# Performance work log

Measured on AMD Instinct MI355X. Metric: run time of the kernel, lower is better.

The kernel has to match this reference:

```python
import jax, jax.numpy as jnp
import numpy as np

THETA = 10000.0
B, S, D, H = 2, 2048, 1024, 16
DK = D // H


def setup_inputs() -> dict:
    key = jax.random.key(0)
    ks = jax.random.split(key, 5)
    std = float(np.sqrt(2.0 / (D + D)))  # get_std(in, out) with in==out==D
    x = jax.random.normal(ks[0], (B, S, D), dtype=jnp.float32)
    Wq = jax.random.normal(ks[1], (D, D), dtype=jnp.float32) * std
    Wk = jax.random.normal(ks[2], (D, D), dtype=jnp.float32) * std
    Wv = jax.random.normal(ks[3], (D, D), dtype=jnp.float32) * std
    Wo = jax.random.normal(ks[4], (D, D), dtype=jnp.float32) * std
    token_positions = jnp.broadcast_to(jnp.arange(S, dtype=jnp.int32), (B, S))
    return {"x": x, "Wq": Wq, "Wk": Wk, "Wv": Wv, "Wo": Wo,
            "token_positions": token_positions}


def _rope(x, pos):
    # x: [B, H, S, d] with interleaved pairs (even=x1, odd=x2); pos: [B, 1, S]
    d = x.shape[-1]
    inv_freq = THETA ** (-(jnp.arange(0, d, 2, dtype=jnp.float32) / d))  # [d/2]
    freqs = pos[..., None].astype(jnp.float32) * inv_freq               # [B,1,S,d/2]
    cos, sin = jnp.cos(freqs), jnp.sin(freqs)
    x1, x2 = x[..., 0::2], x[..., 1::2]
    r1 = cos * x1 - sin * x2
    r2 = sin * x1 + cos * x2
    return jnp.stack([r1, r2], axis=-1).reshape(x.shape)  # re-interleave


def reference(x, Wq, Wk, Wv, Wo, token_positions):
    # Linear is y = x @ W.T (torch weight layout [out, in])
    def split_heads(t):
        return t.reshape(B, S, H, DK).transpose(0, 2, 1, 3)  # [B,H,S,DK]

    Q = split_heads(x @ Wq.T)
    K = split_heads(x @ Wk.T)
    V = split_heads(x @ Wv.T)

    pos = token_positions[:, None, :]  # [B,1,S] broadcast over heads
    Q = _rope(Q, pos)
    K = _rope(K, pos)

    scale = 1.0 / jnp.sqrt(jnp.float32(DK))
    scores = jnp.einsum('bhqd,bhkd->bhqk', Q, K) * scale  # [B,H,S,S]
    causal = jnp.arange(S)[:, None] >= jnp.arange(S)[None, :]
    scores = jnp.where(causal, scores, -jnp.inf)
    weights = jax.nn.softmax(scores, axis=-1)
    attn = jnp.einsum('bhqk,bhkd->bhqd', weights, V)
    attn = attn.transpose(0, 2, 1, 3).reshape(B, S, D)
    return attn @ Wo.T
```

## Files before the change

### kernel.cpp

```cpp
#include <hip/hip_runtime.h>
#include <hip/hip_bf16.h>
#include <math.h>

#define B_ 2
#define S_ 2048
#define D_ 1024
#define H_ 16
#define DK_ 64

typedef __bf16 bf16_t;
typedef bf16_t bf16x8 __attribute__((ext_vector_type(8)));
typedef bf16_t bf16x4 __attribute__((ext_vector_type(4)));
typedef float f32x4 __attribute__((ext_vector_type(4)));

__device__ __forceinline__ void gload16(const void* g, void* lds_base_uniform) {
  __builtin_amdgcn_global_load_lds(
      (const __attribute__((address_space(1))) unsigned int*)g,
      (__attribute__((address_space(3))) unsigned int*)lds_base_uniform, 16, 0, 0);
}

__global__ __launch_bounds__(256) void cast_bf16_vec(const float* __restrict__ in,
                                                     bf16_t* __restrict__ out, int n4) {
  int i = blockIdx.x * 256 + threadIdx.x;
  if (i >= n4) return;
  float4 f = reinterpret_cast<const float4*>(in)[i];
  bf16x4 o;
  o[0] = (bf16_t)f.x; o[1] = (bf16_t)f.y; o[2] = (bf16_t)f.z; o[3] = (bf16_t)f.w;
  reinterpret_cast<bf16x4*>(out)[i] = o;
}

__global__ __launch_bounds__(256) void cast_weights(const float* __restrict__ Wq,
                                                    const float* __restrict__ Wk,
                                                    const float* __restrict__ Wv,
                                                    const float* __restrict__ Wo,
                                                    bf16_t* __restrict__ out) {
  int i = blockIdx.x * 256 + threadIdx.x;
  int r = i >> 18;
  const float* src = (r == 0) ? Wq : (r == 1) ? Wk : (r == 2) ? Wv : Wo;
  float4 f = reinterpret_cast<const float4*>(src)[i & 262143];
  bf16x4 o;
  o[0] = (bf16_t)f.x; o[1] = (bf16_t)f.y; o[2] = (bf16_t)f.z; o[3] = (bf16_t)f.w;
  reinterpret_cast<bf16x4*>(out)[i] = o;
}

template <bool OUT_F32>
__global__ __launch_bounds__(512) void gemm_bt(const bf16_t* __restrict__ A,
                                               const bf16_t* __restrict__ W,
                                               void* __restrict__ Cout,
                                               int Ndim, int Kdim) {
  __shared__ __attribute__((aligned(16))) bf16_t As[128][64];
  __shared__ __attribute__((aligned(16))) bf16_t Bs[128][64];
  const int bm = blockIdx.x * 128;
  const int bn = blockIdx.y * 128;
  const int tid = threadIdx.x;
  const int lane = tid & 63;
  const int w = tid >> 6;
  const int wm = w >> 2, wn = w & 3;
  const int srow_c = lane >> 3;
  const int sslot = lane & 7;

  f32x4 acc[4][2];
  for (int m = 0; m < 4; ++m)
    for (int n = 0; n < 2; ++n) acc[m][n] = (f32x4){0.f, 0.f, 0.f, 0.f};

  for (int k0 = 0; k0 < Kdim; k0 += 64) {
    __syncthreads();
#pragma unroll
    for (int it = 0; it < 2; ++it) {
      const int c = 2 * w + it;
      const int row = c * 8 + srow_c;
      const int col = ((sslot ^ (row & 7)) << 3);
      gload16(&A[(size_t)(bm + row) * Kdim + k0 + col], (char*)&As[0][0] + c * 1024);
      gload16(&W[(size_t)(bn + row) * Kdim + k0 + col], (char*)&Bs[0][0] + c * 1024);
    }
    __syncthreads();
#pragma unroll
    for (int t = 0; t < 2; ++t) {
      const int slot0 = t * 4 + (lane >> 4);
      bf16x8 af[4], bfr[2];
#pragma unroll
      for (int m = 0; m < 4; ++m) {
        const int R = wm * 64 + m * 16 + (lane & 15);
        af[m] = *reinterpret_cast<const bf16x8*>(
            (const char*)&As[0][0] + R * 128 + ((slot0 ^ (R & 7)) << 4));
      }
#pragma unroll
      for (int n = 0; n < 2; ++n) {
        const int R = wn * 32 + n * 16 + (lane & 15);
        bfr[n] = *reinterpret_cast<const bf16x8*>(
            (const char*)&Bs[0][0] + R * 128 + ((slot0 ^ (R & 7)) << 4));
      }
#pragma unroll
      for (int m = 0; m < 4; ++m)
#pragma unroll
        for (int n = 0; n < 2; ++n)
          acc[m][n] = __builtin_amdgcn_mfma_f32_16x16x32_bf16(af[m], bfr[n], acc[m][n], 0, 0, 0);
    }
  }

  const int rg = (lane >> 4) << 2, c0 = lane & 15;
#pragma unroll
  for (int m = 0; m < 4; ++m)
#pragma unroll
    for (int n = 0; n < 2; ++n) {
      int r = bm + wm * 64 + m * 16 + rg;
      int c = bn + wn * 32 + n * 16 + c0;
#pragma unroll
      for (int i = 0; i < 4; ++i) {
        if (OUT_F32)
          reinterpret_cast<float*>(Cout)[(size_t)(r + i) * Ndim + c] = acc[m][n][i];
        else
          reinterpret_cast<bf16_t*>(Cout)[(size_t)(r + i) * Ndim + c] = (bf16_t)acc[m][n][i];
      }
    }
}

__global__ __launch_bounds__(512) void gemm_qkv(const bf16_t* __restrict__ A,
                                                const bf16_t* __restrict__ W,
                                                const int* __restrict__ posids,
                                                bf16_t* __restrict__ Qr,
                                                bf16_t* __restrict__ Kr,
                                                bf16_t* __restrict__ Vt) {
  __shared__ __attribute__((aligned(16))) bf16_t SMEM[2][128][64];
  const int bm = blockIdx.x * 128;
  const int bn = blockIdx.y * 128;
  const int tid = threadIdx.x;
  const int lane = tid & 63;
  const int w = tid >> 6;
  const int wm = w >> 2, wn = w & 3;
  const int srow_c = lane >> 3;
  const int sslot = lane & 7;
  const int Kdim = 1024;

  f32x4 acc[4][2];
  for (int m = 0; m < 4; ++m)
    for (int n = 0; n < 2; ++n) acc[m][n] = (f32x4){0.f, 0.f, 0.f, 0.f};

  for (int k0 = 0; k0 < Kdim; k0 += 64) {
    __syncthreads();
#pragma unroll
    for (int it = 0; it < 2; ++it) {
      const int c = 2 * w + it;
      const int row = c * 8 + srow_c;
      const int col = ((sslot ^ (row & 7)) << 3);
      gload16(&A[(size_t)(bm + row) * Kdim + k0 + col], (char*)&SMEM[0][0][0] + c * 1024);
      gload16(&W[(size_t)(bn + row) * Kdim + k0 + col], (char*)&SMEM[1][0][0] + c * 1024);
    }
    __syncthreads();
#pragma unroll
    for (int t = 0; t < 2; ++t) {
      const int slot0 = t * 4 + (lane >> 4);
      bf16x8 af[4], bfr[2];
#pragma unroll
      for (int m = 0; m < 4; ++m) {
        const int R = wm * 64 + m * 16 + (lane & 15);
        af[m] = *reinterpret_cast<const bf16x8*>(
            (const char*)&SMEM[0][0][0] + R * 128 + ((slot0 ^ (R & 7)) << 4));
      }
#pragma unroll
      for (int n = 0; n < 2; ++n) {
        const int R = wn * 32 + n * 16 + (lane & 15);
        bfr[n] = *reinterpret_cast<const bf16x8*>(
            (const char*)&SMEM[1][0][0] + R * 128 + ((slot0 ^ (R & 7)) << 4));
      }
#pragma unroll
      for (int m = 0; m < 4; ++m)
#pragma unroll
        for (int n = 0; n < 2; ++n)
          acc[m][n] = __builtin_amdgcn_mfma_f32_16x16x32_bf16(af[m], bfr[n], acc[m][n], 0, 0, 0);
    }
  }

  const int region = bn >> 10;
  const int h0 = (bn & 1023) >> 6;
  const int b = bm >> 11;
  const int sblk = bm & 2047;
  char* Cs = (char*)&SMEM[0][0][0];
  const int rg = (lane >> 4) << 2, c0 = lane & 15;

  __syncthreads();

  if (region < 2) {
#pragma unroll
    for (int m = 0; m < 4; ++m)
#pragma unroll
      for (int n = 0; n < 2; ++n) {
        const int col = wn * 32 + n * 16 + c0;
#pragma unroll
        for (int i = 0; i < 4; ++i) {
          const int row = wm * 64 + m * 16 + rg + i;
          *(bf16_t*)(Cs + row * 256 + ((col * 2) ^ ((row & 15) << 4))) = (bf16_t)acc[m][n][i];
        }
      }
    __syncthreads();
    const int sl = tid >> 2;
    const int hh = (tid >> 1) & 1;
    const int jh = tid & 1;
    const int s = sblk + sl;
    const int bh = b * 16 + h0 + hh;
    const int p = posids[b * 2048 + s];
    bf16_t* outp = (region == 0 ? Qr : Kr) + ((size_t)bh * 2048 + s) * 64;
    const float qscale = region == 0 ? 0.125f : 1.0f;
#pragma unroll
    for (int jj = 0; jj < 4; ++jj) {
      const int j = jh * 4 + jj;
      const int slot = hh * 8 + j;
      bf16x8 v = *(const bf16x8*)(Cs + sl * 256 + ((slot ^ (sl & 15)) << 4));
      bf16x8 ov;
#pragma unroll
      for (int e = 0; e < 8; e += 2) {
        const int ii = j * 4 + (e >> 1);
        float sn, cs2;
        __sincosf((float)p * __expf(-(float)(2 * ii) * (9.210340371976184f / 64.0f)),
                  &sn, &cs2);
        const float x1 = (float)v[e], x2 = (float)v[e + 1];
        ov[e]     = (bf16_t)((cs2 * x1 - sn * x2) * qscale);
        ov[e + 1] = (bf16_t)((sn * x1 + cs2 * x2) * qscale);
      }
      *(bf16x8*)(&outp[j * 8]) = ov;
    }
  } else {
#pragma unroll
    for (int m = 0; m < 4; ++m)
#pragma unroll
      for (int n = 0; n < 2; ++n) {
        const int col = wn * 32 + n * 16 + c0;
        const int row0 = wm * 64 + m * 16 + rg;
        bf16x4 pk;
#pragma unroll
        for (int i = 0; i < 4; ++i) pk[i] = (bf16_t)acc[m][n][i];
        *(bf16x4*)(Cs + col * 256 + ((row0 * 2) ^ ((col & 15) << 4))) = pk;
      }
    __syncthreads();
    const int dloc = tid >> 2;
    const int sg2 = (tid >> 1) & 1;
    const int jh = tid & 1;
    const int bh = b * 16 + h0 + (dloc >> 6);
    const int d = dloc & 63;
    bf16_t* outp = Vt + ((size_t)bh * 64 + d) * 2048 + sblk + sg2 * 64;
#pragma unroll
    for (int jj = 0; jj < 4; ++jj) {
      const int j = jh * 4 + jj;
      bf16x8 v = *(const bf16x8*)(Cs + dloc * 256 + (((sg2 * 8 + j) ^ (dloc & 15)) << 4));
      *(bf16x8*)(&outp[j * 8]) = v;
    }
  }
}

__global__ __launch_bounds__(256) void attn_kernel(const bf16_t* __restrict__ Qr,
                                                   const bf16_t* __restrict__ Kr,
                                                   const bf16_t* __restrict__ Vt,
                                                   bf16_t* __restrict__ AO) {
  const int linear = blockIdx.x;
  const int bh = linear & 31;
  const int qt = 31 - (linear >> 5);
  const int b = bh >> 4, h = bh & 15;
  const bf16_t* Qp = Qr + (size_t)bh * S_ * 64;
  const char* Kbase = (const char*)(Kr + (size_t)bh * S_ * 64);
  const char* Vbase = (const char*)(Vt + (size_t)bh * 64 * S_);
  const int tid = threadIdx.x, lane = tid & 63, w = tid >> 6;
  const int qb = qt * 64;
  const int nt = qt + 1;

  __shared__ __attribute__((aligned(16))) bf16_t Ksm[2][64][64];
  __shared__ __attribute__((aligned(16))) bf16_t Vts[2][64][64];
  __shared__ __attribute__((aligned(16))) bf16_t Psm[4][16][64];

  const int srow = lane >> 3;
  const int sslot = lane & 7;

  bf16x8 qf[2];
  {
    int qrow = qb + w * 16 + (lane & 15);
#pragma unroll
    for (int t = 0; t < 2; ++t)
      qf[t] = *reinterpret_cast<const bf16x8*>(
          &Qp[(size_t)qrow * 64 + t * 32 + ((lane >> 4) << 3)]);
  }

  f32x4 o[4];
  for (int m = 0; m < 4; ++m) o[m] = (f32x4){0.f, 0.f, 0.f, 0.f};
  float mrow = -1e30f, lrow = 0.f;

#pragma unroll
  for (int it = 0; it < 2; ++it) {
    int c = 2 * w + it;
    int row = c * 8 + srow;
    gload16(Kbase + (size_t)row * 128 + ((sslot ^ (row & 7)) << 4),
            (char*)&Ksm[0][0][0] + c * 1024);
    gload16(Vbase + (size_t)row * (S_ * 2) + ((sslot ^ (row & 7)) << 4),
            (char*)&Vts[0][0][0] + c * 1024);
  }
  __syncthreads();

  int cur = 0;
#pragma unroll 1
  for (int kt = 0; kt < nt; ++kt) {
    if (kt + 1 < nt) {
#pragma unroll
      for (int it = 0; it < 2; ++it) {
        int c = 2 * w + it;
        int row = c * 8 + srow;
        gload16(Kbase + (size_t)(kt + 1) * 8192 + (size_t)row * 128 + ((sslot ^ (row & 7)) << 4),
                (char*)&Ksm[cur ^ 1][0][0] + c * 1024);
        gload16(Vbase + (size_t)row * (S_ * 2) + (size_t)(kt + 1) * 128 + ((sslot ^ (row & 7)) << 4),
                (char*)&Vts[cur ^ 1][0][0] + c * 1024);
      }
    }

    f32x4 sacc[4];
    for (int m = 0; m < 4; ++m) sacc[m] = (f32x4){0.f, 0.f, 0.f, 0.f};
    __builtin_amdgcn_s_setprio(1);
#pragma unroll
    for (int t = 0; t < 2; ++t) {
      const int slot0 = t * 4 + (lane >> 4);
#pragma unroll
      for (int m = 0; m < 4; ++m) {
        const int R = m * 16 + (lane & 15);
        bf16x8 kfr = *reinterpret_cast<const bf16x8*>(
            (const char*)&Ksm[cur][0][0] + R * 128 + ((slot0 ^ (R & 7)) << 4));
        sacc[m] = __builtin_amdgcn_mfma_f32_16x16x32_bf16(kfr, qf[t], sacc[m], 0, 0, 0);
      }
    }
    __builtin_amdgcn_s_setprio(0);

    const int qrow = qb + w * 16 + (lane & 15);
    const int g4 = (lane >> 4) << 2;
    if (kt * 64 + 63 > qb + w * 16) {
#pragma unroll
      for (int m = 0; m < 4; ++m) {
        const int kc0 = kt * 64 + m * 16 + g4;
#pragma unroll
        for (int r = 0; r < 4; ++r)
          if (kc0 + r > qrow) sacc[m][r] = -1e30f;
      }
    }

    float mx = sacc[0][0];
#pragma unroll
    for (int m = 0; m < 4; ++m)
#pragma unroll
      for (int r = 0; r < 4; ++r) mx = fmaxf(mx, sacc[m][r]);
    mx = fmaxf(mx, __shfl_xor(mx, 16, 64));
    mx = fmaxf(mx, __shfl_xor(mx, 32, 64));
    const float mnew = fmaxf(mrow, mx);
    const float alpha = __expf(mrow - mnew);
    mrow = mnew;

    float s = 0.f;
#pragma unroll
    for (int m = 0; m < 4; ++m)
#pragma unroll
      for (int r = 0; r < 4; ++r) {
        float p = __expf(sacc[m][r] - mnew);
        sacc[m][r] = p;
        s += p;
      }
    s += __shfl_xor(s, 16, 64);
    s += __shfl_xor(s, 32, 64);
    lrow = lrow * alpha + s;

#pragma unroll
    for (int m = 0; m < 4; ++m)
#pragma unroll
      for (int r = 0; r < 4; ++r) o[m][r] *= alpha;

    {
      const int q = lane & 15;
      char* pbase = (char*)&Psm[w][0][0] + q * 128;
      const int xm = (q & 7) << 4;
#pragma unroll
      for (int m = 0; m < 4; ++m) {
        bf16x4 pk;
#pragma unroll
        for (int r = 0; r < 4; ++r) pk[r] = (bf16_t)sacc[m][r];
        *reinterpret_cast<bf16x4*>(pbase + (((m << 5) | ((lane >> 4) << 3)) ^ xm)) = pk;
      }
    }

    __builtin_amdgcn_s_setprio(1);
#pragma unroll
    for (int t = 0; t < 2; ++t) {
      const int slot0 = t * 4 + (lane >> 4);
      bf16x8 pf = *reinterpret_cast<const bf16x8*>(
          (const char*)&Psm[w][0][0] + (lane & 15) * 128 +
          (((t << 6) | ((lane >> 4) << 4)) ^ ((lane & 7) << 4)));
#pragma unroll
      for (int m = 0; m < 4; ++m) {
        const int R = m * 16 + (lane & 15);
        bf16x8 vf = *reinterpret_cast<const bf16x8*>(
            (const char*)&Vts[cur][0][0] + R * 128 + ((slot0 ^ (R & 7)) << 4));
        o[m] = __builtin_amdgcn_mfma_f32_16x16x32_bf16(vf, pf, o[m], 0, 0, 0);
      }
    }
    __builtin_amdgcn_s_setprio(0);

    __syncthreads();
    cur ^= 1;
  }

  {
    const int q = lane & 15;
    const int g4e = (lane >> 4) << 2;
    const int srw = qb + w * 16 + q;
    const float inv = 1.0f / lrow;
#pragma unroll
    for (int m = 0; m < 4; ++m) {
      bf16x4 ov;
#pragma unroll
      for (int r = 0; r < 4; ++r) ov[r] = (bf16_t)(o[m][r] * inv);
      *reinterpret_cast<bf16x4*>(
          &AO[((size_t)(b * S_ + srw)) * 1024 + h * 64 + m * 16 + g4e]) = ov;
    }
  }
}

extern "C" void kernel_launch(void* const* d_in, const int* in_sizes, int n_in,
                              void* d_out, int out_size, void* d_ws, size_t ws_size,
                              hipStream_t stream) {
  const float* x  = (const float*)d_in[0];
  const float* Wq = (const float*)d_in[1];
  const float* Wk = (const float*)d_in[2];
  const float* Wv = (const float*)d_in[3];
  const float* Wo = (const float*)d_in[4];
  const int* tp   = (const int*)d_in[5];

  char* ws = (char*)d_ws;
  bf16_t* xb   = (bf16_t*)(ws);
  bf16_t* Wcat = (bf16_t*)(ws + 8388608);
  bf16_t* Wob  = (bf16_t*)(ws + 14680064);
  bf16_t* Qr   = (bf16_t*)(ws + 41943040);
  bf16_t* Kr   = (bf16_t*)(ws + 50331648);
  bf16_t* Vt   = (bf16_t*)(ws + 58720256);
  bf16_t* AO   = (bf16_t*)(ws + 67108864);

  cast_bf16_vec<<<dim3(4096), dim3(256), 0, stream>>>(x, xb, 1048576);
  cast_weights<<<dim3(4096), dim3(256), 0, stream>>>(Wq, Wk, Wv, Wo, Wcat);

  gemm_qkv<<<dim3(32, 24), dim3(512), 0, stream>>>(xb, Wcat, tp, Qr, Kr, Vt);
  attn_kernel<<<dim3(1024), dim3(256), 0, stream>>>(Qr, Kr, Vt, AO);
  gemm_bt<true><<<dim3(32, 8), dim3(512), 0, stream>>>(AO, Wob, d_out, 1024, 1024);

  (void)in_sizes; (void)n_in; (void)out_size; (void)ws_size;
}
```

Baseline: 118.0 us.

## Use exp2 softmax with lazy rescaling and deferred row-sum reduction

```diff
diff --git a/kernel.cpp b/kernel.cpp
--- a/kernel.cpp
+++ b/kernel.cpp
@@ -17,6 +17,10 @@
   __builtin_amdgcn_global_load_lds(
       (const __attribute__((address_space(1))) unsigned int*)g,
       (__attribute__((address_space(3))) unsigned int*)lds_base_uniform, 16, 0, 0);
+}
+
+__device__ __forceinline__ void drain_ldsdma() {
+  asm volatile("s_waitcnt vmcnt(0)" ::: "memory");
 }
 
 __global__ __launch_bounds__(256) void cast_bf16_vec(const float* __restrict__ in,
@@ -73,6 +77,7 @@
       gload16(&A[(size_t)(bm + row) * Kdim + k0 + col], (char*)&As[0][0] + c * 1024);
       gload16(&W[(size_t)(bn + row) * Kdim + k0 + col], (char*)&Bs[0][0] + c * 1024);
     }
+    drain_ldsdma();
     __syncthreads();
 #pragma unroll
     for (int t = 0; t < 2; ++t) {
@@ -146,6 +151,7 @@
       gload16(&A[(size_t)(bm + row) * Kdim + k0 + col], (char*)&SMEM[0][0][0] + c * 1024);
       gload16(&W[(size_t)(bn + row) * Kdim + k0 + col], (char*)&SMEM[1][0][0] + c * 1024);
     }
+    drain_ldsdma();
     __syncthreads();
 #pragma unroll
     for (int t = 0; t < 2; ++t) {
@@ -200,7 +206,7 @@
     const int bh = b * 16 + h0 + hh;
     const int p = posids[b * 2048 + s];
     bf16_t* outp = (region == 0 ? Qr : Kr) + ((size_t)bh * 2048 + s) * 64;
-    const float qscale = region == 0 ? 0.125f : 1.0f;
+    const float qscale = region == 0 ? 0.18033688011112042f : 1.0f;
 #pragma unroll
     for (int jj = 0; jj < 4; ++jj) {
       const int j = jh * 4 + jj;
@@ -291,6 +297,7 @@
     gload16(Vbase + (size_t)row * (S_ * 2) + ((sslot ^ (row & 7)) << 4),
             (char*)&Vts[0][0][0] + c * 1024);
   }
+  drain_ldsdma();
   __syncthreads();
 
   int cur = 0;
@@ -336,34 +343,35 @@
       }
     }
 
-    float mx = sacc[0][0];
+    float a0 = fmaxf(fmaxf(sacc[0][0], sacc[0][1]), fmaxf(sacc[0][2], sacc[0][3]));
+    float a1 = fmaxf(fmaxf(sacc[1][0], sacc[1][1]), fmaxf(sacc[1][2], sacc[1][3]));
+    float a2 = fmaxf(fmaxf(sacc[2][0], sacc[2][1]), fmaxf(sacc[2][2], sacc[2][3]));
+    float a3 = fmaxf(fmaxf(sacc[3][0], sacc[3][1]), fmaxf(sacc[3][2], sacc[3][3]));
+    float mx = fmaxf(fmaxf(a0, a1), fmaxf(a2, a3));
+
+    if (!__all(mx <= mrow + 4.0f)) {
+      mx = fmaxf(mx, __shfl_xor(mx, 16, 64));
+      mx = fmaxf(mx, __shfl_xor(mx, 32, 64));
+      const float mnew = fmaxf(mrow, mx);
+      const float alpha = __builtin_amdgcn_exp2f(mrow - mnew);
+      mrow = mnew;
+      lrow *= alpha;
+#pragma unroll
+      for (int m = 0; m < 4; ++m)
+#pragma unroll
+        for (int r = 0; r < 4; ++r) o[m][r] *= alpha;
+    }
+
+    float s = 0.f;
 #pragma unroll
     for (int m = 0; m < 4; ++m)
 #pragma unroll
-      for (int r = 0; r < 4; ++r) mx = fmaxf(mx, sacc[m][r]);
-    mx = fmaxf(mx, __shfl_xor(mx, 16, 64));
-    mx = fmaxf(mx, __shfl_xor(mx, 32, 64));
-    const float mnew = fmaxf(mrow, mx);
-    const float alpha = __expf(mrow - mnew);
-    mrow = mnew;
-
-    float s = 0.f;
-#pragma unroll
-    for (int m = 0; m < 4; ++m)
-#pragma unroll
       for (int r = 0; r < 4; ++r) {
-        float p = __expf(sacc[m][r] - mnew);
+        float p = __builtin_amdgcn_exp2f(sacc[m][r] - mrow);
         sacc[m][r] = p;
         s += p;
       }
-    s += __shfl_xor(s, 16, 64);
-    s += __shfl_xor(s, 32, 64);
-    lrow = lrow * alpha + s;
-
-#pragma unroll
-    for (int m = 0; m < 4; ++m)
-#pragma unroll
-      for (int r = 0; r < 4; ++r) o[m][r] *= alpha;
+    lrow += s;
 
     {
       const int q = lane & 15;
@@ -395,11 +403,14 @@
     }
     __builtin_amdgcn_s_setprio(0);
 
+    drain_ldsdma();
     __syncthreads();
     cur ^= 1;
   }
 
   {
+    lrow += __shfl_xor(lrow, 16, 64);
+    lrow += __shfl_xor(lrow, 32, 64);
     const int q = lane & 15;
     const int g4e = (lane >> 4) << 2;
     const int srw = qb + w * 16 + q;
```

Measured after the change: 113.5 us. 3.8% less time.
